# Kernel tuning notes

Hardware: AMD Instinct MI355X
Metric: run time of the kernel (lower is better)

The kernel has to match this reference:

```python
import jax, jax.numpy as jnp
import numpy as np

N = 100000          # nodes
E = 3200000         # edges (avg degree 32)
K = 3               # TAGConv hops
ALPHA = 1.0 / 9.0   # top-k fraction
EPS = 1e-5          # InstanceNorm eps


def setup_inputs() -> dict:
    key = jax.random.key(0)
    ks = jax.random.split(key, 9)
    x = jax.random.uniform(ks[0], (N,), dtype=jnp.float32)
    edge_index = jax.random.randint(ks[1], (2, E), 0, N, dtype=jnp.int64)
    edge_attr = jax.random.normal(ks[2], (E,), dtype=jnp.float32)
    # TAGConv weights: K+1 hop matrices per layer (PyG uses bias once per layer)
    W1 = jax.random.normal(ks[3], (K + 1, 1, 8), dtype=jnp.float32) * 0.5
    b1 = jax.random.normal(ks[4], (8,), dtype=jnp.float32) * 0.1
    W2 = jax.random.normal(ks[5], (K + 1, 8, 8), dtype=jnp.float32) * 0.2
    b2 = jax.random.normal(ks[6], (8,), dtype=jnp.float32) * 0.1
    W3 = jax.random.normal(ks[7], (K + 1, 8, 1), dtype=jnp.float32) * 0.2
    b3 = jax.random.normal(ks[8], (1,), dtype=jnp.float32) * 0.1
    k = int(N * ALPHA)  # 11111
    return {"x": x, "edge_attr": edge_attr, "W1": W1, "b1": b1,
            "W2": W2, "b2": b2, "W3": W3, "b3": b3,
            "edge_index": edge_index, "k": k}


def _tagconv(h, src, dst, norm, W, b):
    # out = sum_{i=0..K} (A_norm^i h) @ W[i] + b
    out = h @ W[0]
    for i in range(1, W.shape[0]):
        h = jax.ops.segment_sum(norm[:, None] * h[src], dst, num_segments=N)
        out = out + h @ W[i]
    return out + b


def reference(x, edge_attr, W1, b1, W2, b2, W3, b3, edge_index, k):
    src, dst = edge_index[0], edge_index[1]
    w = jnp.abs(edge_attr)
    # gcn_norm without self-loops (PyG TAGConv default)
    deg = jax.ops.segment_sum(w, dst, num_segments=N)
    deg_safe = jnp.where(deg > 0, deg, 1.0)
    dinv = jnp.where(deg > 0, jax.lax.rsqrt(deg_safe), 0.0)
    norm = dinv[src] * w * dinv[dst]

    h = x[:, None]  # [N, 1]
    h = jax.nn.relu(_tagconv(h, src, dst, norm, W1, b1))
    h = jax.nn.relu(_tagconv(h, src, dst, norm, W2, b2))
    h = jax.nn.relu(_tagconv(h, src, dst, norm, W3, b3))

    # InstanceNorm(1): normalize over nodes per channel (biased var, no affine)
    mu = jnp.mean(h, axis=0)
    var = jnp.mean((h - mu) ** 2, axis=0)
    h = ((h - mu) * jax.lax.rsqrt(var + EPS))[:, 0]  # [N]

    # diff_top_k
    order = jnp.argsort(-h)
    topk = order[:k]
    top_k_vec = jnp.full((N,), -1.0, dtype=h.dtype).at[topk].set(1.0)
    k_smallest = jnp.abs(h[topk[k - 1]])
    soft = jax.nn.sigmoid(h - k_smallest + top_k_vec * 0.1)

    return jnp.stack([h, soft], axis=1)  # [N, 2]
```

## Files before the change

### kernel.cpp

```cpp
#include <hip/hip_runtime.h>
#include <math.h>

#define NN 100000
#define NE 3200000

static constexpr int TPB = 256;
static constexpr int GRID_E = (NE + TPB - 1) / TPB;
static constexpr int GRID_N = (NN + TPB - 1) / TPB;
static constexpr int GRID_N4 = (NN * 4 + TPB - 1) / TPB;

__global__ void k_init(const int* __restrict__ kptr, unsigned* __restrict__ prefix,
                       int* __restrict__ target, int* __restrict__ cgt,
                       double* __restrict__ stats) {
  *prefix = 0u;
  *target = *kptr;
  *cgt = 0;
  stats[0] = 0.0;
  stats[1] = 0.0;
}

__global__ void k_cnt(const int* __restrict__ dst, int* __restrict__ cnt,
                      int* __restrict__ ppos) {
  int e = blockIdx.x * TPB + threadIdx.x;
  if (e >= NE) return;
  ppos[e] = atomicAdd(&cnt[dst[e]], 1);
}

__global__ void k_bsum(const int* __restrict__ cnt, int* __restrict__ bsum) {
  __shared__ int sh[TPB];
  int t = threadIdx.x;
  int i = blockIdx.x * TPB + t;
  sh[t] = (i < NN) ? cnt[i] : 0;
  __syncthreads();
  for (int o = TPB / 2; o > 0; o >>= 1) {
    if (t < o) sh[t] += sh[t + o];
    __syncthreads();
  }
  if (t == 0) bsum[blockIdx.x] = sh[0];
}

__global__ void k_bscan(const int* __restrict__ bsum, int* __restrict__ bpre,
                        int* __restrict__ rowptr) {
  if (threadIdx.x == 0) {
    int acc = 0;
    for (int b = 0; b < GRID_N; ++b) { bpre[b] = acc; acc += bsum[b]; }
    rowptr[NN] = NE;
  }
}

__global__ void k_rowptr(const int* __restrict__ cnt, const int* __restrict__ bpre,
                         int* __restrict__ rowptr) {
  __shared__ int sh[TPB];
  int t = threadIdx.x;
  int i = blockIdx.x * TPB + t;
  int v = (i < NN) ? cnt[i] : 0;
  sh[t] = v;
  __syncthreads();
  for (int o = 1; o < TPB; o <<= 1) {
    int a = (t >= o) ? sh[t - o] : 0;
    __syncthreads();
    sh[t] += a;
    __syncthreads();
  }
  if (i < NN) rowptr[i] = sh[t] - v + bpre[blockIdx.x];
}

__global__ void k_scatter(const int* __restrict__ src, const int* __restrict__ dst,
                          const float* __restrict__ ea, const int* __restrict__ ppos,
                          const int* __restrict__ rowptr, int2* __restrict__ ed) {
  int e = blockIdx.x * TPB + threadIdx.x;
  if (e >= NE) return;
  int d = dst[e];
  ed[rowptr[d] + ppos[e]] = make_int2(src[e], __float_as_int(fabsf(ea[e])));
}

__global__ void g_degdinv(const int* __restrict__ rowptr, const int2* __restrict__ ed,
                          float* __restrict__ dinv) {
  int t = blockIdx.x * TPB + threadIdx.x;
  int n = t >> 2, r = t & 3;
  if (n >= NN) return;
  int s0 = rowptr[n], s1 = rowptr[n + 1];
  float acc = 0.0f;
  for (int i = s0 + r; i < s1; i += 4) acc += __int_as_float(ed[i].y);
  acc += __shfl_xor(acc, 1);
  acc += __shfl_xor(acc, 2);
  if (r == 0) dinv[n] = (acc > 0.0f) ? (1.0f / sqrtf(acc)) : 0.0f;
}

__global__ void g_prop1fix(const int* __restrict__ rowptr, int2* __restrict__ ed,
                           const float* __restrict__ dinv, const float* __restrict__ hin,
                           float* __restrict__ hout) {
  int t = blockIdx.x * TPB + threadIdx.x;
  int n = t >> 2, r = t & 3;
  if (n >= NN) return;
  int s0 = rowptr[n], s1 = rowptr[n + 1];
  float dn = dinv[n];
  float acc = 0.0f;
  for (int i = s0 + r; i < s1; i += 4) {
    int2 e = ed[i];
    float w = __int_as_float(e.y) * dinv[e.x] * dn;
    ed[i].y = __float_as_int(w);
    acc += w * hin[e.x];
  }
  acc += __shfl_xor(acc, 1);
  acc += __shfl_xor(acc, 2);
  if (r == 0) hout[n] = acc;
}

__global__ void g_prop1(const int* __restrict__ rowptr, const int2* __restrict__ ed,
                        const float* __restrict__ hin, float* __restrict__ hout) {
  int t = blockIdx.x * TPB + threadIdx.x;
  int n = t >> 2, r = t & 3;
  if (n >= NN) return;
  int s0 = rowptr[n], s1 = rowptr[n + 1];
  float acc = 0.0f;
  for (int i = s0 + r; i < s1; i += 4) {
    int2 e = ed[i];
    acc += __int_as_float(e.y) * hin[e.x];
  }
  acc += __shfl_xor(acc, 1);
  acc += __shfl_xor(acc, 2);
  if (r == 0) hout[n] = acc;
}

__global__ void g_prop1c(const int* __restrict__ rowptr, const int2* __restrict__ ed,
                         const float* __restrict__ x, const float* __restrict__ p1,
                         const float* __restrict__ p2, const float* __restrict__ hin,
                         const float* __restrict__ W, const float* __restrict__ b,
                         float* __restrict__ out) {
  int t = blockIdx.x * TPB + threadIdx.x;
  int n = t >> 2, r = t & 3;
  if (n >= NN) return;
  int s0 = rowptr[n], s1 = rowptr[n + 1];
  float acc = 0.0f;
  for (int i = s0 + r; i < s1; i += 4) {
    int2 e = ed[i];
    acc += __int_as_float(e.y) * hin[e.x];
  }
  acc += __shfl_xor(acc, 1);
  acc += __shfl_xor(acc, 2);
  if (r == 0) {
    float h0 = x[n], h1 = p1[n], h2 = p2[n], h3 = acc;
    float* op = out + (size_t)n * 8;
    #pragma unroll
    for (int j = 0; j < 8; ++j) {
      float v = b[j] + h0 * W[j] + h1 * W[8 + j] + h2 * W[16 + j] + h3 * W[24 + j];
      op[j] = fmaxf(v, 0.0f);
    }
  }
}

__global__ void g_prop8(const int* __restrict__ rowptr, const int2* __restrict__ ed,
                        const float* __restrict__ hin, float* __restrict__ hout) {
  int t = blockIdx.x * TPB + threadIdx.x;
  int n = t >> 2, r = t & 3;
  if (n >= NN) return;
  int s0 = rowptr[n], s1 = rowptr[n + 1];
  float a0 = 0, a1 = 0, a2 = 0, a3 = 0, a4 = 0, a5 = 0, a6 = 0, a7 = 0;
  for (int i = s0 + r; i < s1; i += 4) {
    int2 e = ed[i];
    float w = __int_as_float(e.y);
    const float4* hp = (const float4*)(hin + (size_t)e.x * 8);
    float4 xx = hp[0], yy = hp[1];
    a0 += w * xx.x; a1 += w * xx.y; a2 += w * xx.z; a3 += w * xx.w;
    a4 += w * yy.x; a5 += w * yy.y; a6 += w * yy.z; a7 += w * yy.w;
  }
  #pragma unroll
  for (int m = 1; m <= 2; m <<= 1) {
    a0 += __shfl_xor(a0, m); a1 += __shfl_xor(a1, m);
    a2 += __shfl_xor(a2, m); a3 += __shfl_xor(a3, m);
    a4 += __shfl_xor(a4, m); a5 += __shfl_xor(a5, m);
    a6 += __shfl_xor(a6, m); a7 += __shfl_xor(a7, m);
  }
  if (r == 0) {
    float4* op = (float4*)(hout + (size_t)n * 8);
    op[0] = make_float4(a0, a1, a2, a3);
    op[1] = make_float4(a4, a5, a6, a7);
  }
}

__global__ void g_prop8c8(const int* __restrict__ rowptr, const int2* __restrict__ ed,
                          const float* __restrict__ p0, const float* __restrict__ p1,
                          const float* __restrict__ hin,
                          const float* __restrict__ W, const float* __restrict__ b,
                          float* __restrict__ out) {
  int t = blockIdx.x * TPB + threadIdx.x;
  int n = t >> 2, r = t & 3;
  if (n >= NN) return;
  int s0 = rowptr[n], s1 = rowptr[n + 1];
  float a0 = 0, a1 = 0, a2 = 0, a3 = 0, a4 = 0, a5 = 0, a6 = 0, a7 = 0;
  for (int i = s0 + r; i < s1; i += 4) {
    int2 e = ed[i];
    float w = __int_as_float(e.y);
    const float4* hp = (const float4*)(hin + (size_t)e.x * 8);
    float4 xx = hp[0], yy = hp[1];
    a0 += w * xx.x; a1 += w * xx.y; a2 += w * xx.z; a3 += w * xx.w;
    a4 += w * yy.x; a5 += w * yy.y; a6 += w * yy.z; a7 += w * yy.w;
  }
  #pragma unroll
  for (int m = 1; m <= 2; m <<= 1) {
    a0 += __shfl_xor(a0, m); a1 += __shfl_xor(a1, m);
    a2 += __shfl_xor(a2, m); a3 += __shfl_xor(a3, m);
    a4 += __shfl_xor(a4, m); a5 += __shfl_xor(a5, m);
    a6 += __shfl_xor(a6, m); a7 += __shfl_xor(a7, m);
  }
  if (r == 0) {
    float h[4][8];
    const float4* hp = (const float4*)(p0 + (size_t)n * 8);
    float4 u = hp[0], v4 = hp[1];
    h[0][0]=u.x; h[0][1]=u.y; h[0][2]=u.z; h[0][3]=u.w; h[0][4]=v4.x; h[0][5]=v4.y; h[0][6]=v4.z; h[0][7]=v4.w;
    hp = (const float4*)(p1 + (size_t)n * 8);
    u = hp[0]; v4 = hp[1];
    h[1][0]=u.x; h[1][1]=u.y; h[1][2]=u.z; h[1][3]=u.w; h[1][4]=v4.x; h[1][5]=v4.y; h[1][6]=v4.z; h[1][7]=v4.w;
    hp = (const float4*)(hin + (size_t)n * 8);
    u = hp[0]; v4 = hp[1];
    h[2][0]=u.x; h[2][1]=u.y; h[2][2]=u.z; h[2][3]=u.w; h[2][4]=v4.x; h[2][5]=v4.y; h[2][6]=v4.z; h[2][7]=v4.w;
    h[3][0]=a0; h[3][1]=a1; h[3][2]=a2; h[3][3]=a3; h[3][4]=a4; h[3][5]=a5; h[3][6]=a6; h[3][7]=a7;
    float* op = out + (size_t)n * 8;
    #pragma unroll
    for (int j = 0; j < 8; ++j) {
      float v = b[j];
      #pragma unroll
      for (int i = 0; i < 4; ++i) {
        #pragma unroll
        for (int f = 0; f < 8; ++f) v += h[i][f] * W[i * 64 + f * 8 + j];
      }
      op[j] = fmaxf(v, 0.0f);
    }
  }
}

__global__ void g_prop8c3(const int* __restrict__ rowptr, const int2* __restrict__ ed,
                          const float* __restrict__ p0, const float* __restrict__ p1,
                          const float* __restrict__ hin,
                          const float* __restrict__ W, const float* __restrict__ b,
                          float* __restrict__ out) {
  int t = blockIdx.x * TPB + threadIdx.x;
  int n = t >> 2, r = t & 3;
  if (n >= NN) return;
  int s0 = rowptr[n], s1 = rowptr[n + 1];
  float a0 = 0, a1 = 0, a2 = 0, a3 = 0, a4 = 0, a5 = 0, a6 = 0, a7 = 0;
  for (int i = s0 + r; i < s1; i += 4) {
    int2 e = ed[i];
    float w = __int_as_float(e.y);
    const float4* hp = (const float4*)(hin + (size_t)e.x * 8);
    float4 xx = hp[0], yy = hp[1];
    a0 += w * xx.x; a1 += w * xx.y; a2 += w * xx.z; a3 += w * xx.w;
    a4 += w * yy.x; a5 += w * yy.y; a6 += w * yy.z; a7 += w * yy.w;
  }
  #pragma unroll
  for (int m = 1; m <= 2; m <<= 1) {
    a0 += __shfl_xor(a0, m); a1 += __shfl_xor(a1, m);
    a2 += __shfl_xor(a2, m); a3 += __shfl_xor(a3, m);
    a4 += __shfl_xor(a4, m); a5 += __shfl_xor(a5, m);
    a6 += __shfl_xor(a6, m); a7 += __shfl_xor(a7, m);
  }
  if (r == 0) {
    float v = b[0];
    const float4* hp = (const float4*)(p0 + (size_t)n * 8);
    float4 u = hp[0], w4 = hp[1];
    v += u.x*W[0] + u.y*W[1] + u.z*W[2] + u.w*W[3] + w4.x*W[4] + w4.y*W[5] + w4.z*W[6] + w4.w*W[7];
    hp = (const float4*)(p1 + (size_t)n * 8);
    u = hp[0]; w4 = hp[1];
    v += u.x*W[8] + u.y*W[9] + u.z*W[10] + u.w*W[11] + w4.x*W[12] + w4.y*W[13] + w4.z*W[14] + w4.w*W[15];
    hp = (const float4*)(hin + (size_t)n * 8);
    u = hp[0]; w4 = hp[1];
    v += u.x*W[16] + u.y*W[17] + u.z*W[18] + u.w*W[19] + w4.x*W[20] + w4.y*W[21] + w4.z*W[22] + w4.w*W[23];
    v += a0*W[24] + a1*W[25] + a2*W[26] + a3*W[27] + a4*W[28] + a5*W[29] + a6*W[30] + a7*W[31];
    out[n] = fmaxf(v, 0.0f);
  }
}


__global__ void k_stats(const float* __restrict__ h, double* __restrict__ stats) {
  int n = blockIdx.x * TPB + threadIdx.x;
  float v = (n < NN) ? h[n] : 0.0f;
  double s = (double)v, s2 = (double)v * (double)v;
  #pragma unroll
  for (int o = 32; o > 0; o >>= 1) {
    s  += __shfl_down(s, o);
    s2 += __shfl_down(s2, o);
  }
  __shared__ double ls[4], ls2[4];
  int lane = threadIdx.x & 63, w = threadIdx.x >> 6;
  if (lane == 0) { ls[w] = s; ls2[w] = s2; }
  __syncthreads();
  if (threadIdx.x == 0) {
    atomicAdd(&stats[0], ls[0] + ls[1] + ls[2] + ls[3]);
    atomicAdd(&stats[1], ls2[0] + ls2[1] + ls2[2] + ls2[3]);
  }
}

__global__ void k_normkey(const float* __restrict__ h, const double* __restrict__ stats,
                          float* __restrict__ hn, unsigned* __restrict__ key) {
  int n = blockIdx.x * TPB + threadIdx.x;
  if (n >= NN) return;
  double mu = stats[0] / (double)NN;
  double var = stats[1] / (double)NN - mu * mu;
  if (var < 0.0) var = 0.0;
  double invs = 1.0 / sqrt(var + 1e-5);
  float v = (float)(((double)h[n] - mu) * invs);
  hn[n] = v;
  unsigned u = __float_as_uint(v);
  unsigned asc = (u & 0x80000000u) ? ~u : (u | 0x80000000u);
  key[n] = ~asc;
}

template <int SHIFT, unsigned MASK>
__global__ void k_hist(const unsigned* __restrict__ key, const unsigned* __restrict__ prefix,
                       unsigned* __restrict__ hist) {
  __shared__ unsigned lh[256];
  lh[threadIdx.x] = 0;
  __syncthreads();
  int n = blockIdx.x * TPB + threadIdx.x;
  unsigned pfx = *prefix;
  if (n < NN) {
    unsigned kk = key[n];
    if ((kk & MASK) == pfx) atomicAdd(&lh[(kk >> SHIFT) & 0xffu], 1u);
  }
  __syncthreads();
  if (lh[threadIdx.x]) atomicAdd(&hist[threadIdx.x], lh[threadIdx.x]);
}

template <int SHIFT>
__global__ void k_pick(const unsigned* __restrict__ hist, unsigned* __restrict__ prefix,
                       int* __restrict__ target) {
  int t = *target;
  unsigned cum = 0;
  for (int b = 0; b < 256; ++b) {
    unsigned c = hist[b];
    if ((int)(cum + c) >= t) {
      *prefix |= ((unsigned)b) << SHIFT;
      *target = t - (int)cum;
      return;
    }
    cum += c;
  }
}

__global__ void k_count(const unsigned* __restrict__ key, const unsigned* __restrict__ prefix,
                        int* __restrict__ partials, int* __restrict__ cgt) {
  int n = blockIdx.x * TPB + threadIdx.x;
  unsigned T = *prefix;
  bool eq = false, lt = false;
  if (n < NN) {
    unsigned kk = key[n];
    eq = (kk == T);
    lt = (kk < T);
  }
  unsigned long long meq = __ballot(eq);
  unsigned long long mlt = __ballot(lt);
  __shared__ int ce[4], cl[4];
  int lane = threadIdx.x & 63, w = threadIdx.x >> 6;
  if (lane == 0) { ce[w] = __popcll(meq); cl[w] = __popcll(mlt); }
  __syncthreads();
  if (threadIdx.x == 0) {
    partials[blockIdx.x] = ce[0] + ce[1] + ce[2] + ce[3];
    int l = cl[0] + cl[1] + cl[2] + cl[3];
    if (l) atomicAdd(cgt, l);
  }
}

__global__ void k_scan(const int* __restrict__ partials, int* __restrict__ offs,
                       const int* __restrict__ kptr, const int* __restrict__ cgt,
                       int* __restrict__ r) {
  if (threadIdx.x == 0) {
    int acc = 0;
    for (int b = 0; b < GRID_N; ++b) { offs[b] = acc; acc += partials[b]; }
    *r = *kptr - *cgt;
  }
}

__global__ void k_final(const float* __restrict__ hn, const unsigned* __restrict__ key,
                        const unsigned* __restrict__ prefix, const int* __restrict__ offs,
                        const int* __restrict__ rptr, float* __restrict__ out) {
  int n = blockIdx.x * TPB + threadIdx.x;
  unsigned T = *prefix;
  int r = *rptr;
  bool eq = false, lt = false;
  float v = 0.0f;
  if (n < NN) {
    unsigned kk = key[n];
    eq = (kk == T);
    lt = (kk < T);
    v = hn[n];
  }
  unsigned long long m = __ballot(eq);
  __shared__ int wc[4];
  int lane = threadIdx.x & 63, w = threadIdx.x >> 6;
  if (lane == 0) wc[w] = __popcll(m);
  __syncthreads();
  int off = offs[blockIdx.x];
  for (int i = 0; i < w; ++i) off += wc[i];
  off += __popcll(m & ((1ull << lane) - 1ull));
  if (n >= NN) return;
  bool top = lt || (eq && off < r);
  unsigned asc = ~T;
  unsigned orig = (asc & 0x80000000u) ? (asc & 0x7fffffffu) : ~asc;
  float thr = fabsf(__uint_as_float(orig));
  float tkv = top ? 1.0f : -1.0f;
  float z = v - thr + tkv * 0.1f;
  out[2 * n]     = v;
  out[2 * n + 1] = 1.0f / (1.0f + expf(-z));
}

extern "C" void kernel_launch(void* const* d_in, const int* in_sizes, int n_in,
                              void* d_out, int out_size, void* d_ws, size_t ws_size,
                              hipStream_t stream) {
  const float* x       = (const float*)d_in[0];
  const float* ea      = (const float*)d_in[1];
  const float* W1      = (const float*)d_in[2];
  const float* b1      = (const float*)d_in[3];
  const float* W2      = (const float*)d_in[4];
  const float* b2      = (const float*)d_in[5];
  const float* W3      = (const float*)d_in[6];
  const float* b3      = (const float*)d_in[7];
  const int* ei        = (const int*)d_in[8];
  const int* kptr      = (const int*)d_in[9];
  float* out           = (float*)d_out;

  const int* src = ei;
  const int* dst = ei + NE;

  char* ws = (char*)d_ws;
  size_t off = 0;
  auto alloc = [&](size_t bytes) -> void* {
    void* p = ws + off;
    off += (bytes + 255) & ~(size_t)255;
    return p;
  };

  int2*     ed       = (int2*)alloc((size_t)NE * 8);
  int*      ppos     = (int*)alloc((size_t)NE * 4);
  int*      cnt      = (int*)alloc((size_t)NN * 4);
  int*      rowptr   = (int*)alloc(((size_t)NN + 1) * 4);
  int*      bsum     = (int*)alloc(512 * 4);
  int*      bpre     = (int*)alloc(512 * 4);
  float*    dinv     = (float*)alloc((size_t)NN * 4);
  float*    pA       = (float*)alloc((size_t)NN * 8 * 4);
  float*    pB       = (float*)alloc((size_t)NN * 8 * 4);
  float*    h1       = (float*)alloc((size_t)NN * 8 * 4);
  float*    h2       = (float*)alloc((size_t)NN * 8 * 4);
  float*    h3       = (float*)alloc((size_t)NN * 4);
  float*    hn       = (float*)alloc((size_t)NN * 4);
  unsigned* key      = (unsigned*)alloc((size_t)NN * 4);
  double*   stats    = (double*)alloc(2 * 8);
  unsigned* hist     = (unsigned*)alloc(256 * 4);
  int*      partials = (int*)alloc(512 * 4);
  int*      offs     = (int*)alloc(512 * 4);
  unsigned* prefix   = (unsigned*)alloc(4);
  int*      target   = (int*)alloc(4);
  int*      cgt      = (int*)alloc(4);
  int*      rr       = (int*)alloc(4);

  k_init<<<1, 1, 0, stream>>>(kptr, prefix, target, cgt, stats);

  hipMemsetAsync(cnt, 0, (size_t)NN * 4, stream);
  k_cnt<<<GRID_E, TPB, 0, stream>>>(dst, cnt, ppos);
  k_bsum<<<GRID_N, TPB, 0, stream>>>(cnt, bsum);
  k_bscan<<<1, 64, 0, stream>>>(bsum, bpre, rowptr);
  k_rowptr<<<GRID_N, TPB, 0, stream>>>(cnt, bpre, rowptr);
  k_scatter<<<GRID_E, TPB, 0, stream>>>(src, dst, ea, ppos, rowptr, ed);

  g_degdinv<<<GRID_N4, TPB, 0, stream>>>(rowptr, ed, dinv);

  g_prop1fix<<<GRID_N4, TPB, 0, stream>>>(rowptr, ed, dinv, x, pA);
  g_prop1<<<GRID_N4, TPB, 0, stream>>>(rowptr, ed, pA, pB);
  g_prop1c<<<GRID_N4, TPB, 0, stream>>>(rowptr, ed, x, pA, pB, pB, W1, b1, h1);

  g_prop8<<<GRID_N4, TPB, 0, stream>>>(rowptr, ed, h1, pA);
  g_prop8<<<GRID_N4, TPB, 0, stream>>>(rowptr, ed, pA, pB);
  g_prop8c8<<<GRID_N4, TPB, 0, stream>>>(rowptr, ed, h1, pA, pB, W2, b2, h2);

  g_prop8<<<GRID_N4, TPB, 0, stream>>>(rowptr, ed, h2, pA);
  g_prop8<<<GRID_N4, TPB, 0, stream>>>(rowptr, ed, pA, pB);
  g_prop8c3<<<GRID_N4, TPB, 0, stream>>>(rowptr, ed, h2, pA, pB, W3, b3, h3);

  k_stats<<<GRID_N, TPB, 0, stream>>>(h3, stats);
  k_normkey<<<GRID_N, TPB, 0, stream>>>(h3, stats, hn, key);

  hipMemsetAsync(hist, 0, 1024, stream);
  k_hist<24, 0x00000000u><<<GRID_N, TPB, 0, stream>>>(key, prefix, hist);
  k_pick<24><<<1, 1, 0, stream>>>(hist, prefix, target);
  hipMemsetAsync(hist, 0, 1024, stream);
  k_hist<16, 0xFF000000u><<<GRID_N, TPB, 0, stream>>>(key, prefix, hist);
  k_pick<16><<<1, 1, 0, stream>>>(hist, prefix, target);
  hipMemsetAsync(hist, 0, 1024, stream);
  k_hist<8, 0xFFFF0000u><<<GRID_N, TPB, 0, stream>>>(key, prefix, hist);
  k_pick<8><<<1, 1, 0, stream>>>(hist, prefix, target);
  hipMemsetAsync(hist, 0, 1024, stream);
  k_hist<0, 0xFFFFFF00u><<<GRID_N, TPB, 0, stream>>>(key, prefix, hist);
  k_pick<0><<<1, 1, 0, stream>>>(hist, prefix, target);

  k_count<<<GRID_N, TPB, 0, stream>>>(key, prefix, partials, cgt);
  k_scan<<<1, 64, 0, stream>>>(partials, offs, kptr, cgt, rr);
  k_final<<<GRID_N, TPB, 0, stream>>>(hn, key, prefix, offs, rr, out);
}
```

Before: 710.7 us.

## Reassociate layer-3 TAGConv to scalar Horner propagation; split degree counters

Layer 3 has one output channel, so its weights are applied to the layer-2 output inside the fused layer-2 combine kernel. The three 8-wide propagations of layer 3 become three scalar Horner-style propagations (u = A s3 + s2, v = A u + s1, h3 = relu(A v + g0)), which cuts the gather traffic of those passes roughly eightfold. Degree counting spreads its atomics over four sub-histograms chosen by block index to reduce contention, at the cost of an extra combine kernel and more memory. The top-k rank bookkeeping drops the less-than counter and passes the remaining target from radix select straight to the final kernel. The reassociation changes the order of floating-point summation.

```diff
diff --git a/kernel.cpp b/kernel.cpp
--- a/kernel.cpp
+++ b/kernel.cpp
@@ -3,6 +3,7 @@
 
 #define NN 100000
 #define NE 3200000
+#define NSUB 4
 
 static constexpr int TPB = 256;
 static constexpr int GRID_E = (NE + TPB - 1) / TPB;
@@ -10,11 +11,9 @@
 static constexpr int GRID_N4 = (NN * 4 + TPB - 1) / TPB;
 
 __global__ void k_init(const int* __restrict__ kptr, unsigned* __restrict__ prefix,
-                       int* __restrict__ target, int* __restrict__ cgt,
-                       double* __restrict__ stats) {
+                       int* __restrict__ target, double* __restrict__ stats) {
   *prefix = 0u;
   *target = *kptr;
-  *cgt = 0;
   stats[0] = 0.0;
   stats[1] = 0.0;
 }
@@ -23,14 +22,26 @@
                       int* __restrict__ ppos) {
   int e = blockIdx.x * TPB + threadIdx.x;
   if (e >= NE) return;
-  ppos[e] = atomicAdd(&cnt[dst[e]], 1);
-}
-
-__global__ void k_bsum(const int* __restrict__ cnt, int* __restrict__ bsum) {
+  int sub = blockIdx.x & (NSUB - 1);
+  ppos[e] = atomicAdd(&cnt[sub * NN + dst[e]], 1);
+}
+
+__global__ void k_tot(int* __restrict__ cnt, int* __restrict__ tot) {
+  int n = blockIdx.x * TPB + threadIdx.x;
+  if (n >= NN) return;
+  int c0 = cnt[n], c1 = cnt[NN + n], c2 = cnt[2 * NN + n], c3 = cnt[3 * NN + n];
+  cnt[n] = 0;
+  cnt[NN + n] = c0;
+  cnt[2 * NN + n] = c0 + c1;
+  cnt[3 * NN + n] = c0 + c1 + c2;
+  tot[n] = c0 + c1 + c2 + c3;
+}
+
+__global__ void k_bsum(const int* __restrict__ tot, int* __restrict__ bsum) {
   __shared__ int sh[TPB];
   int t = threadIdx.x;
   int i = blockIdx.x * TPB + t;
-  sh[t] = (i < NN) ? cnt[i] : 0;
+  sh[t] = (i < NN) ? tot[i] : 0;
   __syncthreads();
   for (int o = TPB / 2; o > 0; o >>= 1) {
     if (t < o) sh[t] += sh[t + o];
@@ -48,12 +59,12 @@
   }
 }
 
-__global__ void k_rowptr(const int* __restrict__ cnt, const int* __restrict__ bpre,
+__global__ void k_rowptr(const int* __restrict__ tot, const int* __restrict__ bpre,
                          int* __restrict__ rowptr) {
   __shared__ int sh[TPB];
   int t = threadIdx.x;
   int i = blockIdx.x * TPB + t;
-  int v = (i < NN) ? cnt[i] : 0;
+  int v = (i < NN) ? tot[i] : 0;
   sh[t] = v;
   __syncthreads();
   for (int o = 1; o < TPB; o <<= 1) {
@@ -67,11 +78,14 @@
 
 __global__ void k_scatter(const int* __restrict__ src, const int* __restrict__ dst,
                           const float* __restrict__ ea, const int* __restrict__ ppos,
-                          const int* __restrict__ rowptr, int2* __restrict__ ed) {
+                          const int* __restrict__ rowptr, const int* __restrict__ cnt,
+                          int2* __restrict__ ed) {
   int e = blockIdx.x * TPB + threadIdx.x;
   if (e >= NE) return;
+  int sub = blockIdx.x & (NSUB - 1);
   int d = dst[e];
-  ed[rowptr[d] + ppos[e]] = make_int2(src[e], __float_as_int(fabsf(ea[e])));
+  int pos = rowptr[d] + cnt[sub * NN + d] + ppos[e];
+  ed[pos] = make_int2(src[e], __float_as_int(fabsf(ea[e])));
 }
 
 __global__ void g_degdinv(const int* __restrict__ rowptr, const int2* __restrict__ ed,
@@ -121,6 +135,27 @@
   acc += __shfl_xor(acc, 1);
   acc += __shfl_xor(acc, 2);
   if (r == 0) hout[n] = acc;
+}
+
+template <int RELU>
+__global__ void g_prop1add(const int* __restrict__ rowptr, const int2* __restrict__ ed,
+                           const float* __restrict__ gsrc, const float* __restrict__ addv,
+                           float* __restrict__ out) {
+  int t = blockIdx.x * TPB + threadIdx.x;
+  int n = t >> 2, r = t & 3;
+  if (n >= NN) return;
+  int s0 = rowptr[n], s1 = rowptr[n + 1];
+  float acc = 0.0f;
+  for (int i = s0 + r; i < s1; i += 4) {
+    int2 e = ed[i];
+    acc += __int_as_float(e.y) * gsrc[e.x];
+  }
+  acc += __shfl_xor(acc, 1);
+  acc += __shfl_xor(acc, 2);
+  if (r == 0) {
+    float v = addv[n] + acc;
+    out[n] = RELU ? fmaxf(v, 0.0f) : v;
+  }
 }
 
 __global__ void g_prop1c(const int* __restrict__ rowptr, const int2* __restrict__ ed,
@@ -179,11 +214,13 @@
   }
 }
 
-__global__ void g_prop8c8(const int* __restrict__ rowptr, const int2* __restrict__ ed,
+__global__ void g_prop8l3(const int* __restrict__ rowptr, const int2* __restrict__ ed,
                           const float* __restrict__ p0, const float* __restrict__ p1,
                           const float* __restrict__ hin,
-                          const float* __restrict__ W, const float* __restrict__ b,
-                          float* __restrict__ out) {
+                          const float* __restrict__ W2, const float* __restrict__ b2,
+                          const float* __restrict__ W3, const float* __restrict__ b3,
+                          float* __restrict__ g0o, float* __restrict__ s1o,
+                          float* __restrict__ s2o, float* __restrict__ s3o) {
   int t = blockIdx.x * TPB + threadIdx.x;
   int n = t >> 2, r = t & 3;
   if (n >= NN) return;
@@ -216,61 +253,28 @@
     u = hp[0]; v4 = hp[1];
     h[2][0]=u.x; h[2][1]=u.y; h[2][2]=u.z; h[2][3]=u.w; h[2][4]=v4.x; h[2][5]=v4.y; h[2][6]=v4.z; h[2][7]=v4.w;
     h[3][0]=a0; h[3][1]=a1; h[3][2]=a2; h[3][3]=a3; h[3][4]=a4; h[3][5]=a5; h[3][6]=a6; h[3][7]=a7;
-    float* op = out + (size_t)n * 8;
+    float hv[8];
     #pragma unroll
     for (int j = 0; j < 8; ++j) {
-      float v = b[j];
+      float v = b2[j];
       #pragma unroll
       for (int i = 0; i < 4; ++i) {
         #pragma unroll
-        for (int f = 0; f < 8; ++f) v += h[i][f] * W[i * 64 + f * 8 + j];
+        for (int f = 0; f < 8; ++f) v += h[i][f] * W2[i * 64 + f * 8 + j];
       }
-      op[j] = fmaxf(v, 0.0f);
+      hv[j] = fmaxf(v, 0.0f);
     }
-  }
-}
-
-__global__ void g_prop8c3(const int* __restrict__ rowptr, const int2* __restrict__ ed,
-                          const float* __restrict__ p0, const float* __restrict__ p1,
-                          const float* __restrict__ hin,
-                          const float* __restrict__ W, const float* __restrict__ b,
-                          float* __restrict__ out) {
-  int t = blockIdx.x * TPB + threadIdx.x;
-  int n = t >> 2, r = t & 3;
-  if (n >= NN) return;
-  int s0 = rowptr[n], s1 = rowptr[n + 1];
-  float a0 = 0, a1 = 0, a2 = 0, a3 = 0, a4 = 0, a5 = 0, a6 = 0, a7 = 0;
-  for (int i = s0 + r; i < s1; i += 4) {
-    int2 e = ed[i];
-    float w = __int_as_float(e.y);
-    const float4* hp = (const float4*)(hin + (size_t)e.x * 8);
-    float4 xx = hp[0], yy = hp[1];
-    a0 += w * xx.x; a1 += w * xx.y; a2 += w * xx.z; a3 += w * xx.w;
-    a4 += w * yy.x; a5 += w * yy.y; a6 += w * yy.z; a7 += w * yy.w;
-  }
-  #pragma unroll
-  for (int m = 1; m <= 2; m <<= 1) {
-    a0 += __shfl_xor(a0, m); a1 += __shfl_xor(a1, m);
-    a2 += __shfl_xor(a2, m); a3 += __shfl_xor(a3, m);
-    a4 += __shfl_xor(a4, m); a5 += __shfl_xor(a5, m);
-    a6 += __shfl_xor(a6, m); a7 += __shfl_xor(a7, m);
-  }
-  if (r == 0) {
-    float v = b[0];
-    const float4* hp = (const float4*)(p0 + (size_t)n * 8);
-    float4 u = hp[0], w4 = hp[1];
-    v += u.x*W[0] + u.y*W[1] + u.z*W[2] + u.w*W[3] + w4.x*W[4] + w4.y*W[5] + w4.z*W[6] + w4.w*W[7];
-    hp = (const float4*)(p1 + (size_t)n * 8);
-    u = hp[0]; w4 = hp[1];
-    v += u.x*W[8] + u.y*W[9] + u.z*W[10] + u.w*W[11] + w4.x*W[12] + w4.y*W[13] + w4.z*W[14] + w4.w*W[15];
-    hp = (const float4*)(hin + (size_t)n * 8);
-    u = hp[0]; w4 = hp[1];
-    v += u.x*W[16] + u.y*W[17] + u.z*W[18] + u.w*W[19] + w4.x*W[20] + w4.y*W[21] + w4.z*W[22] + w4.w*W[23];
-    v += a0*W[24] + a1*W[25] + a2*W[26] + a3*W[27] + a4*W[28] + a5*W[29] + a6*W[30] + a7*W[31];
-    out[n] = fmaxf(v, 0.0f);
-  }
-}
-
+    float g0 = b3[0], sv1 = 0, sv2 = 0, sv3 = 0;
+    #pragma unroll
+    for (int f = 0; f < 8; ++f) {
+      g0  += hv[f] * W3[f];
+      sv1 += hv[f] * W3[8 + f];
+      sv2 += hv[f] * W3[16 + f];
+      sv3 += hv[f] * W3[24 + f];
+    }
+    g0o[n] = g0; s1o[n] = sv1; s2o[n] = sv2; s3o[n] = sv3;
+  }
+}
 
 __global__ void k_stats(const float* __restrict__ h, double* __restrict__ stats) {
   int n = blockIdx.x * TPB + threadIdx.x;
@@ -339,35 +343,22 @@
 }
 
 __global__ void k_count(const unsigned* __restrict__ key, const unsigned* __restrict__ prefix,
-                        int* __restrict__ partials, int* __restrict__ cgt) {
+                        int* __restrict__ partials) {
   int n = blockIdx.x * TPB + threadIdx.x;
   unsigned T = *prefix;
-  bool eq = false, lt = false;
-  if (n < NN) {
-    unsigned kk = key[n];
-    eq = (kk == T);
-    lt = (kk < T);
-  }
+  bool eq = (n < NN) && (key[n] == T);
   unsigned long long meq = __ballot(eq);
-  unsigned long long mlt = __ballot(lt);
-  __shared__ int ce[4], cl[4];
+  __shared__ int ce[4];
   int lane = threadIdx.x & 63, w = threadIdx.x >> 6;
-  if (lane == 0) { ce[w] = __popcll(meq); cl[w] = __popcll(mlt); }
-  __syncthreads();
-  if (threadIdx.x == 0) {
-    partials[blockIdx.x] = ce[0] + ce[1] + ce[2] + ce[3];
-    int l = cl[0] + cl[1] + cl[2] + cl[3];
-    if (l) atomicAdd(cgt, l);
-  }
-}
-
-__global__ void k_scan(const int* __restrict__ partials, int* __restrict__ offs,
-                       const int* __restrict__ kptr, const int* __restrict__ cgt,
-                       int* __restrict__ r) {
+  if (lane == 0) ce[w] = __popcll(meq);
+  __syncthreads();
+  if (threadIdx.x == 0) partials[blockIdx.x] = ce[0] + ce[1] + ce[2] + ce[3];
+}
+
+__global__ void k_scan(const int* __restrict__ partials, int* __restrict__ offs) {
   if (threadIdx.x == 0) {
     int acc = 0;
     for (int b = 0; b < GRID_N; ++b) { offs[b] = acc; acc += partials[b]; }
-    *r = *kptr - *cgt;
   }
 }
 
@@ -432,7 +423,8 @@
 
   int2*     ed       = (int2*)alloc((size_t)NE * 8);
   int*      ppos     = (int*)alloc((size_t)NE * 4);
-  int*      cnt      = (int*)alloc((size_t)NN * 4);
+  int*      cnt      = (int*)alloc((size_t)NSUB * NN * 4);
+  int*      tot      = (int*)alloc((size_t)NN * 4);
   int*      rowptr   = (int*)alloc(((size_t)NN + 1) * 4);
   int*      bsum     = (int*)alloc(512 * 4);
   int*      bpre     = (int*)alloc(512 * 4);
@@ -440,7 +432,12 @@
   float*    pA       = (float*)alloc((size_t)NN * 8 * 4);
   float*    pB       = (float*)alloc((size_t)NN * 8 * 4);
   float*    h1       = (float*)alloc((size_t)NN * 8 * 4);
-  float*    h2       = (float*)alloc((size_t)NN * 8 * 4);
+  float*    g0       = (float*)alloc((size_t)NN * 4);
+  float*    s1       = (float*)alloc((size_t)NN * 4);
+  float*    s2       = (float*)alloc((size_t)NN * 4);
+  float*    s3       = (float*)alloc((size_t)NN * 4);
+  float*    u        = (float*)alloc((size_t)NN * 4);
+  float*    v        = (float*)alloc((size_t)NN * 4);
   float*    h3       = (float*)alloc((size_t)NN * 4);
   float*    hn       = (float*)alloc((size_t)NN * 4);
   unsigned* key      = (unsigned*)alloc((size_t)NN * 4);
@@ -450,17 +447,16 @@
   int*      offs     = (int*)alloc(512 * 4);
   unsigned* prefix   = (unsigned*)alloc(4);
   int*      target   = (int*)alloc(4);
-  int*      cgt      = (int*)alloc(4);
-  int*      rr       = (int*)alloc(4);
-
-  k_init<<<1, 1, 0, stream>>>(kptr, prefix, target, cgt, stats);
-
-  hipMemsetAsync(cnt, 0, (size_t)NN * 4, stream);
+
+  k_init<<<1, 1, 0, stream>>>(kptr, prefix, target, stats);
+
+  hipMemsetAsync(cnt, 0, (size_t)NSUB * NN * 4, stream);
   k_cnt<<<GRID_E, TPB, 0, stream>>>(dst, cnt, ppos);
-  k_bsum<<<GRID_N, TPB, 0, stream>>>(cnt, bsum);
+  k_tot<<<GRID_N, TPB, 0, stream>>>(cnt, tot);
+  k_bsum<<<GRID_N, TPB, 0, stream>>>(tot, bsum);
   k_bscan<<<1, 64, 0, stream>>>(bsum, bpre, rowptr);
-  k_rowptr<<<GRID_N, TPB, 0, stream>>>(cnt, bpre, rowptr);
-  k_scatter<<<GRID_E, TPB, 0, stream>>>(src, dst, ea, ppos, rowptr, ed);
+  k_rowptr<<<GRID_N, TPB, 0, stream>>>(tot, bpre, rowptr);
+  k_scatter<<<GRID_E, TPB, 0, stream>>>(src, dst, ea, ppos, rowptr, cnt, ed);
 
   g_degdinv<<<GRID_N4, TPB, 0, stream>>>(rowptr, ed, dinv);
 
@@ -470,11 +466,12 @@
 
   g_prop8<<<GRID_N4, TPB, 0, stream>>>(rowptr, ed, h1, pA);
   g_prop8<<<GRID_N4, TPB, 0, stream>>>(rowptr, ed, pA, pB);
-  g_prop8c8<<<GRID_N4, TPB, 0, stream>>>(rowptr, ed, h1, pA, pB, W2, b2, h2);
-
-  g_prop8<<<GRID_N4, TPB, 0, stream>>>(rowptr, ed, h2, pA);
-  g_prop8<<<GRID_N4, TPB, 0, stream>>>(rowptr, ed, pA, pB);
-  g_prop8c3<<<GRID_N4, TPB, 0, stream>>>(rowptr, ed, h2, pA, pB, W3, b3, h3);
+  g_prop8l3<<<GRID_N4, TPB, 0, stream>>>(rowptr, ed, h1, pA, pB, W2, b2, W3, b3,
+                                         g0, s1, s2, s3);
+
+  g_prop1add<0><<<GRID_N4, TPB, 0, stream>>>(rowptr, ed, s3, s2, u);
+  g_prop1add<0><<<GRID_N4, TPB, 0, stream>>>(rowptr, ed, u, s1, v);
+  g_prop1add<1><<<GRID_N4, TPB, 0, stream>>>(rowptr, ed, v, g0, h3);
 
   k_stats<<<GRID_N, TPB, 0, stream>>>(h3, stats);
   k_normkey<<<GRID_N, TPB, 0, stream>>>(h3, stats, hn, key);
@@ -492,7 +489,7 @@
   k_hist<0, 0xFFFFFF00u><<<GRID_N, TPB, 0, stream>>>(key, prefix, hist);
   k_pick<0><<<1, 1, 0, stream>>>(hist, prefix, target);
 
-  k_count<<<GRID_N, TPB, 0, stream>>>(key, prefix, partials, cgt);
-  k_scan<<<1, 64, 0, stream>>>(partials, offs, kptr, cgt, rr);
-  k_final<<<GRID_N, TPB, 0, stream>>>(hn, key, prefix, offs, rr, out);
-}
+  k_count<<<GRID_N, TPB, 0, stream>>>(key, prefix, partials);
+  k_scan<<<1, 64, 0, stream>>>(partials, offs);
+  k_final<<<GRID_N, TPB, 0, stream>>>(hn, key, prefix, offs, target, out);
+}
```

New measurement: 670.1 us. 1.06x faster.
